# Performance work log

Hardware: AMD Instinct MI355X
Metric: run time of the kernel (lower is better)

Reference implementation:

```python
import jax, jax.numpy as jnp
import numpy as np

B, D, C, L, H = 4096, 768, 512, 32, 256
E = C * L  # total flattened extension embeddings

def _l2norm(x, eps=1e-12):
    n = jnp.sqrt(jnp.sum(x * x, axis=-1, keepdims=True))
    return x / jnp.maximum(n, eps)

def setup_inputs() -> dict:
    key = jax.random.key(0)
    ks = jax.random.split(key, 8)
    text_feat = jax.random.normal(ks[0], (B, D), dtype=jnp.float32)
    img_feat = jax.random.normal(ks[1], (B, D), dtype=jnp.float32)
    ext_embs = _l2norm(jax.random.normal(ks[2], (E, D), dtype=jnp.float32))
    concept_names = _l2norm(jax.random.normal(ks[3], (C, D), dtype=jnp.float32))
    # each concept has exactly L extension embeddings; sorted segment ids
    segment_ids = jnp.repeat(jnp.arange(C, dtype=jnp.int32), L)
    W1 = jax.random.normal(ks[4], (C + D, H), dtype=jnp.float32) * (1.0 / np.sqrt(C + D))
    b1 = jnp.zeros((H,), dtype=jnp.float32)
    W2 = jax.random.normal(ks[5], (H, C), dtype=jnp.float32) * (1.0 / np.sqrt(H))
    b2 = jnp.zeros((C,), dtype=jnp.float32)
    alpha = jnp.float32(0.5)
    temperature = jnp.float32(0.07)
    return {"text_feat": text_feat, "img_feat": img_feat, "ext_embs": ext_embs,
            "segment_ids": segment_ids, "concept_names": concept_names,
            "W1": W1, "b1": b1, "W2": W2, "b2": b2,
            "alpha": alpha, "temperature": temperature}

def reference(text_feat, img_feat, ext_embs, segment_ids, concept_names,
              W1, b1, W2, b2, alpha, temperature):
    # query = normalize(text + img)
    q = _l2norm(text_feat + img_feat)                      # [B, D]
    # ragged per-concept max similarity: one big GEMM + segmented max
    sim = jnp.einsum('bd,ed->be', q, ext_embs)            # [B, E]
    prior = jax.ops.segment_max(sim.T, segment_ids,
                                num_segments=C,
                                indices_are_sorted=True).T  # [B, C]
    # small MLP -> temperature softmax -> weighted concept sum
    h = jax.nn.relu(jnp.concatenate([prior, q], axis=-1) @ W1 + b1)  # [B, H]
    logits = h @ W2 + b2                                   # [B, C]
    weights = jax.nn.softmax(logits / temperature, axis=-1)
    dyn_prompt = weights @ concept_names                   # [B, D]
    combined = text_feat + alpha * dyn_prompt
    return _l2norm(combined)
```

## Files before the change

### kernel.cpp

```cpp
#include <hip/hip_runtime.h>
#include <hip/hip_bf16.h>

typedef unsigned short bfu;
typedef __attribute__((ext_vector_type(4))) float f32x4;
typedef __attribute__((ext_vector_type(8))) short bf16x8;
typedef __attribute__((ext_vector_type(4))) int i32x4;
typedef __attribute__((ext_vector_type(8))) int i32x8;

#define GAS __attribute__((address_space(1)))
#define LAS __attribute__((address_space(3)))

__device__ __forceinline__ unsigned short f2bf(float f) {
    unsigned int u = __float_as_uint(f);
    u += 0x7FFFu + ((u >> 16) & 1u);
    return (unsigned short)(u >> 16);
}

__device__ __forceinline__ void gld_lds16(const void* g, void* l) {
    __builtin_amdgcn_global_load_lds((GAS void*)g, (LAS void*)l, 16, 0, 0);
}

__device__ __forceinline__ unsigned pack_fp8x4(float a, float b, float c, float d) {
    int u = __builtin_amdgcn_cvt_pk_fp8_f32(a, b, 0, false);
    u = __builtin_amdgcn_cvt_pk_fp8_f32(c, d, u, true);
    return (unsigned)u;
}

__device__ __forceinline__ float block_sum256(float v, float* sm) {
    #pragma unroll
    for (int off = 32; off; off >>= 1) v += __shfl_xor(v, off);
    int w = threadIdx.x >> 6;
    if ((threadIdx.x & 63) == 0) sm[w] = v;
    __syncthreads();
    float r = sm[0] + sm[1] + sm[2] + sm[3];
    __syncthreads();
    return r;
}

__device__ __forceinline__ float block_max256(float v, float* sm) {
    #pragma unroll
    for (int off = 32; off; off >>= 1) v = fmaxf(v, __shfl_xor(v, off));
    int w = threadIdx.x >> 6;
    if ((threadIdx.x & 63) == 0) sm[w] = v;
    __syncthreads();
    float r = fmaxf(fmaxf(sm[0], sm[1]), fmaxf(sm[2], sm[3]));
    __syncthreads();
    return r;
}

__global__ __launch_bounds__(256) void prep_kernel(const float* __restrict__ text,
                                                   const float* __restrict__ img,
                                                   bfu* __restrict__ X,
                                                   unsigned* __restrict__ Q8,
                                                   const float* __restrict__ ext,
                                                   unsigned* __restrict__ E8,
                                                   const float* __restrict__ W1, bfu* __restrict__ W1t,
                                                   const float* __restrict__ W2, bfu* __restrict__ W2t,
                                                   const float* __restrict__ cn, bfu* __restrict__ cnt) {
    __shared__ float sm[4];
    int b = blockIdx.x, t = threadIdx.x;
    if (b < 4096) {
        int row = b;
        float4 v = {0.f, 0.f, 0.f, 0.f};
        if (t < 192) {
            float4 a = ((const float4*)(text + (size_t)row * 768))[t];
            float4 c = ((const float4*)(img + (size_t)row * 768))[t];
            v.x = a.x + c.x; v.y = a.y + c.y; v.z = a.z + c.z; v.w = a.w + c.w;
        }
        float ss = v.x * v.x + v.y * v.y + v.z * v.z + v.w * v.w;
        float tot = block_sum256(ss, sm);
        float inv = 1.0f / fmaxf(sqrtf(tot), 1e-12f);
        if (t < 192) {
            ushort4 o = make_ushort4(f2bf(v.x * inv), f2bf(v.y * inv), f2bf(v.z * inv), f2bf(v.w * inv));
            ((ushort4*)(X + (size_t)row * 1280 + 512))[t] = o;
            float s16 = inv * 16.0f;
            Q8[(size_t)row * 192 + t] = pack_fp8x4(v.x * s16, v.y * s16, v.z * s16, v.w * s16);
        }
    } else if (b < 16384) {
        int i = (b - 4096) * 256 + t;
        float4 v = ((const float4*)ext)[i];
        E8[i] = pack_fp8x4(v.x * 16.0f, v.y * 16.0f, v.z * 16.0f, v.w * 16.0f);
    } else if (b < 17664) {
        int idx = (b - 16384) * 256 + t;
        int c = idx / 1280, r = idx - c * 1280;
        W1t[idx] = f2bf(W1[(size_t)r * 256 + c]);
    } else if (b < 18176) {
        int idx = (b - 17664) * 256 + t;
        int c = idx / 256, r = idx - c * 256;
        W2t[idx] = f2bf(W2[(size_t)r * 512 + c]);
    } else {
        int idx = (b - 18176) * 256 + t;
        int c = idx / 512, r = idx - c * 512;
        cnt[idx] = f2bf(cn[(size_t)r * 768 + c]);
    }
}

__device__ __forceinline__ i32x8 ld_frag8(const char* s, int row, int lq) {
    const int r7 = row & 7;
    i32x4 lo = *(const i32x4*)(s + row * 128 + ((((lq << 1))     ^ r7) << 4));
    i32x4 hi = *(const i32x4*)(s + row * 128 + ((((lq << 1) | 1) ^ r7) << 4));
    i32x8 v;
    v[0] = lo[0]; v[1] = lo[1]; v[2] = lo[2]; v[3] = lo[3];
    v[4] = hi[0]; v[5] = hi[1]; v[6] = hi[2]; v[7] = hi[3];
    return v;
}

__global__ __launch_bounds__(256) void sim_segmax_kernel(const unsigned char* __restrict__ Q8,
                                                         const unsigned char* __restrict__ E8,
                                                         bfu* __restrict__ X) {
    __shared__ __align__(16) char sA[128 * 128];
    __shared__ __align__(16) char sB[128 * 128];
    int xcd = blockIdx.x & 7;
    int lid = blockIdx.x >> 3;
    int bm = lid & 31;
    int bn = ((lid >> 5) << 3) | xcd;
    int m0 = bm * 128, n0 = bn * 128;
    const int t = threadIdx.x, lane = t & 63, wv = t >> 6;
    const int wm = (wv >> 1) << 6, wn = (wv & 1) << 6;
    const int lr = lane & 15, lq = lane >> 4;

    f32x4 zero = {0.f, 0.f, 0.f, 0.f};
    f32x4 acc[4][4];
    #pragma unroll
    for (int i = 0; i < 4; ++i)
        #pragma unroll
        for (int j = 0; j < 4; ++j) acc[i][j] = zero;

    for (int k0 = 0; k0 < 768; k0 += 128) {
        #pragma unroll
        for (int i = 0; i < 4; ++i) {
            int idx = i * 256 + t;
            int row = idx >> 3, cs = idx & 7, cg = cs ^ (row & 7);
            gld_lds16(Q8 + (size_t)(m0 + row) * 768 + k0 + (cg << 4), sA + idx * 16);
            gld_lds16(E8 + (size_t)(n0 + row) * 768 + k0 + (cg << 4), sB + idx * 16);
        }
        __syncthreads();
        i32x8 af[4], bf8[4];
        #pragma unroll
        for (int f = 0; f < 4; ++f) {
            af[f]  = ld_frag8(sA, wm + f * 16 + lr, lq);
            bf8[f] = ld_frag8(sB, wn + f * 16 + lr, lq);
        }
        #pragma unroll
        for (int i = 0; i < 4; ++i)
            #pragma unroll
            for (int j = 0; j < 4; ++j)
                acc[i][j] = __builtin_amdgcn_mfma_scale_f32_16x16x128_f8f6f4(
                    af[i], bf8[j], acc[i][j], 0, 0, 0, 0x7F7F7F7F, 0, 0x7F7F7F7F);
        __syncthreads();
    }

    const float sc = 0.00390625f;
    #pragma unroll
    for (int i = 0; i < 4; ++i) {
        #pragma unroll
        for (int r = 0; r < 4; ++r) {
            float g0 = fmaxf(acc[i][0][r], acc[i][1][r]);
            float g1 = fmaxf(acc[i][2][r], acc[i][3][r]);
            #pragma unroll
            for (int off = 8; off; off >>= 1) {
                g0 = fmaxf(g0, __shfl_xor(g0, off));
                g1 = fmaxf(g1, __shfl_xor(g1, off));
            }
            if (lr == 0) {
                int row = m0 + wm + i * 16 + lq * 4 + r;
                int g = (n0 + wn) >> 5;
                X[(size_t)row * 1280 + g]     = f2bf(g0 * sc);
                X[(size_t)row * 1280 + g + 1] = f2bf(g1 * sc);
            }
        }
    }
}

template <int BM>
__device__ __forceinline__ void gemm_mainloop(const bfu* A, const bfu* B, int K,
                                              int lda, int ldb, int m0, int n0,
                                              short* sA, short* sB, f32x4 acc[BM / 32][4]) {
    const int t = threadIdx.x, lane = t & 63, wv = t >> 6;
    const int wm = (wv >> 1) * (BM / 2), wn = (wv & 1) << 6;
    const int lr = lane & 15, lq = lane >> 4;

    for (int k0 = 0; k0 < K; k0 += 64) {
        #pragma unroll
        for (int i = 0; i < BM / 32; ++i) {
            int idx = i * 256 + t;
            int row = idx >> 3, cs = idx & 7, cg = cs ^ (row & 7);
            gld_lds16(A + (size_t)(m0 + row) * lda + k0 + (cg << 3), sA + idx * 8);
        }
        #pragma unroll
        for (int i = 0; i < 4; ++i) {
            int idx = i * 256 + t;
            int row = idx >> 3, cs = idx & 7, cg = cs ^ (row & 7);
            gld_lds16(B + (size_t)(n0 + row) * ldb + k0 + (cg << 3), sB + idx * 8);
        }
        __syncthreads();
        #pragma unroll
        for (int kk = 0; kk < 2; ++kk) {
            bf16x8 af[BM / 32], bfr[4];
            #pragma unroll
            for (int f = 0; f < BM / 32; ++f) {
                int mrow = wm + f * 16 + lr;
                int c = kk * 4 + lq;
                af[f] = *(const bf16x8*)(sA + mrow * 64 + ((c ^ (mrow & 7)) << 3));
            }
            #pragma unroll
            for (int f = 0; f < 4; ++f) {
                int nrow = wn + f * 16 + lr;
                int c = kk * 4 + lq;
                bfr[f] = *(const bf16x8*)(sB + nrow * 64 + ((c ^ (nrow & 7)) << 3));
            }
            #pragma unroll
            for (int i = 0; i < BM / 32; ++i)
                #pragma unroll
                for (int j = 0; j < 4; ++j)
                    acc[i][j] = __builtin_amdgcn_mfma_f32_16x16x32_bf16(af[i], bfr[j], acc[i][j], 0, 0, 0);
        }
        __syncthreads();
    }
}

template <int EPI, int BM>
__global__ __launch_bounds__(256) void gemm_kernel(const bfu* __restrict__ A,
                                                   const bfu* __restrict__ B,
                                                   const float* __restrict__ bias,
                                                   void* __restrict__ out,
                                                   int K, int lda, int ldb, int N, int ntN) {
    __shared__ __align__(16) short sA[BM * 64];
    __shared__ __align__(16) short sB[128 * 64];
    int bm = blockIdx.x / ntN, bn = blockIdx.x - bm * ntN;
    int m0 = bm * BM, n0 = bn * 128;
    f32x4 zero = {0.f, 0.f, 0.f, 0.f};
    f32x4 acc[BM / 32][4];
    #pragma unroll
    for (int i = 0; i < BM / 32; ++i)
        #pragma unroll
        for (int j = 0; j < 4; ++j) acc[i][j] = zero;

    gemm_mainloop<BM>(A, B, K, lda, ldb, m0, n0, sA, sB, acc);

    const int t = threadIdx.x, lane = t & 63, wv = t >> 6;
    const int wm = (wv >> 1) * (BM / 2), wn = (wv & 1) << 6;
    const int lr = lane & 15, lq = lane >> 4;
    #pragma unroll
    for (int j = 0; j < 4; ++j) {
        int col = n0 + wn + j * 16 + lr;
        float bv = (EPI >= 1) ? bias[col] : 0.0f;
        #pragma unroll
        for (int i = 0; i < BM / 32; ++i) {
            #pragma unroll
            for (int r = 0; r < 4; ++r) {
                int row = m0 + wm + i * 16 + lq * 4 + r;
                float v = acc[i][j][r] + bv;
                if (EPI == 1) {
                    v = fmaxf(v, 0.0f);
                    ((bfu*)out)[(size_t)row * N + col] = f2bf(v);
                } else {
                    ((float*)out)[(size_t)row * N + col] = v;
                }
            }
        }
    }
}

__global__ __launch_bounds__(256) void softmax_kernel(const float* __restrict__ logits,
                                                      const float* __restrict__ temp,
                                                      bfu* __restrict__ wout) {
    __shared__ float sm[4];
    int row = blockIdx.x, t = threadIdx.x;
    float invT = 1.0f / temp[0];
    float l0 = logits[(size_t)row * 512 + t];
    float l1 = logits[(size_t)row * 512 + 256 + t];
    float m = block_max256(fmaxf(l0, l1), sm);
    float e0 = __expf((l0 - m) * invT);
    float e1 = __expf((l1 - m) * invT);
    float s = block_sum256(e0 + e1, sm);
    float inv = 1.0f / s;
    wout[(size_t)row * 512 + t]       = f2bf(e0 * inv);
    wout[(size_t)row * 512 + 256 + t] = f2bf(e1 * inv);
}

__global__ __launch_bounds__(256) void final_kernel(const float* __restrict__ text,
                                                    const float* __restrict__ dyn,
                                                    const float* __restrict__ alpha,
                                                    float* __restrict__ out) {
    __shared__ float sm[4];
    int row = blockIdx.x, t = threadIdx.x;
    float a = alpha[0];
    float v[3]; float ss = 0.f;
    #pragma unroll
    for (int i = 0; i < 3; ++i) {
        size_t o = (size_t)row * 768 + t + 256 * i;
        v[i] = text[o] + a * dyn[o];
        ss += v[i] * v[i];
    }
    float tot = block_sum256(ss, sm);
    float inv = 1.0f / fmaxf(sqrtf(tot), 1e-12f);
    #pragma unroll
    for (int i = 0; i < 3; ++i)
        out[(size_t)row * 768 + t + 256 * i] = v[i] * inv;
}

extern "C" void kernel_launch(void* const* d_in, const int* in_sizes, int n_in,
                              void* d_out, int out_size, void* d_ws, size_t ws_size,
                              hipStream_t stream) {
    const float* text  = (const float*)d_in[0];
    const float* img   = (const float*)d_in[1];
    const float* ext   = (const float*)d_in[2];
    const float* cn    = (const float*)d_in[4];
    const float* W1    = (const float*)d_in[5];
    const float* b1    = (const float*)d_in[6];
    const float* W2    = (const float*)d_in[7];
    const float* b2    = (const float*)d_in[8];
    const float* alpha = (const float*)d_in[9];
    const float* temp  = (const float*)d_in[10];
    float* out = (float*)d_out;

    char* p = (char*)d_ws;
    auto carve = [&](size_t bytes) -> char* {
        char* r = p; p += (bytes + 255) & ~(size_t)255; return r;
    };
    unsigned char* E8 = (unsigned char*)carve((size_t)16384 * 768);
    unsigned char* Q8 = (unsigned char*)carve((size_t)4096 * 768);
    bfu*   X      = (bfu*)carve((size_t)4096 * 1280 * 2);
    bfu*   W1t    = (bfu*)carve((size_t)256 * 1280 * 2);
    bfu*   W2t    = (bfu*)carve((size_t)512 * 256 * 2);
    bfu*   cnt    = (bfu*)carve((size_t)768 * 512 * 2);
    bfu*   Hm     = (bfu*)carve((size_t)4096 * 256 * 2);
    float* logits = (float*)carve((size_t)4096 * 512 * 4);
    bfu*   wts    = (bfu*)carve((size_t)4096 * 512 * 2);
    float* dyn    = (float*)carve((size_t)4096 * 768 * 4);

    prep_kernel<<<19712, 256, 0, stream>>>(text, img, X, (unsigned*)Q8,
                                           ext, (unsigned*)E8, W1, W1t, W2, W2t, cn, cnt);
    sim_segmax_kernel<<<4096, 256, 0, stream>>>(Q8, E8, X);
    gemm_kernel<1, 32><<<128 * 2, 256, 0, stream>>>(X, W1t, b1, (void*)Hm, 1280, 1280, 1280, 256, 2);
    gemm_kernel<2, 32><<<128 * 4, 256, 0, stream>>>(Hm, W2t, b2, (void*)logits, 256, 256, 256, 512, 4);
    softmax_kernel<<<4096, 256, 0, stream>>>(logits, temp, wts);
    gemm_kernel<0, 32><<<128 * 6, 256, 0, stream>>>(wts, cnt, nullptr, (void*)dyn, 512, 512, 512, 768, 6);
    final_kernel<<<4096, 256, 0, stream>>>(text, dyn, alpha, out);
}
```

Baseline: 314.9 us.

## Prefetch GEMM tiles through registers instead of direct global-to-LDS loads

```diff
diff --git a/kernel.cpp b/kernel.cpp
--- a/kernel.cpp
+++ b/kernel.cpp
@@ -7,17 +7,10 @@
 typedef __attribute__((ext_vector_type(4))) int i32x4;
 typedef __attribute__((ext_vector_type(8))) int i32x8;
 
-#define GAS __attribute__((address_space(1)))
-#define LAS __attribute__((address_space(3)))
-
 __device__ __forceinline__ unsigned short f2bf(float f) {
     unsigned int u = __float_as_uint(f);
     u += 0x7FFFu + ((u >> 16) & 1u);
     return (unsigned short)(u >> 16);
-}
-
-__device__ __forceinline__ void gld_lds16(const void* g, void* l) {
-    __builtin_amdgcn_global_load_lds((GAS void*)g, (LAS void*)l, 16, 0, 0);
 }
 
 __device__ __forceinline__ unsigned pack_fp8x4(float a, float b, float c, float d) {
@@ -110,10 +103,8 @@
                                                          bfu* __restrict__ X) {
     __shared__ __align__(16) char sA[128 * 128];
     __shared__ __align__(16) char sB[128 * 128];
-    int xcd = blockIdx.x & 7;
-    int lid = blockIdx.x >> 3;
-    int bm = lid & 31;
-    int bn = ((lid >> 5) << 3) | xcd;
+    int bm = blockIdx.x >> 7;
+    int bn = blockIdx.x & 127;
     int m0 = bm * 128, n0 = bn * 128;
     const int t = threadIdx.x, lane = t & 63, wv = t >> 6;
     const int wm = (wv >> 1) << 6, wn = (wv & 1) << 6;
@@ -126,15 +117,32 @@
         #pragma unroll
         for (int j = 0; j < 4; ++j) acc[i][j] = zero;
 
-    for (int k0 = 0; k0 < 768; k0 += 128) {
+    i32x4 ra[4], rb[4];
+    auto ldg = [&](int k0) {
         #pragma unroll
         for (int i = 0; i < 4; ++i) {
             int idx = i * 256 + t;
-            int row = idx >> 3, cs = idx & 7, cg = cs ^ (row & 7);
-            gld_lds16(Q8 + (size_t)(m0 + row) * 768 + k0 + (cg << 4), sA + idx * 16);
-            gld_lds16(E8 + (size_t)(n0 + row) * 768 + k0 + (cg << 4), sB + idx * 16);
-        }
+            int row = idx >> 3, cg = idx & 7;
+            ra[i] = *(const i32x4*)(Q8 + (size_t)(m0 + row) * 768 + k0 + (cg << 4));
+            rb[i] = *(const i32x4*)(E8 + (size_t)(n0 + row) * 768 + k0 + (cg << 4));
+        }
+    };
+    auto st_lds = [&]() {
+        #pragma unroll
+        for (int i = 0; i < 4; ++i) {
+            int idx = i * 256 + t;
+            int row = idx >> 3, cg = idx & 7, cs = cg ^ (row & 7);
+            *(i32x4*)(sA + (row * 8 + cs) * 16) = ra[i];
+            *(i32x4*)(sB + (row * 8 + cs) * 16) = rb[i];
+        }
+    };
+
+    ldg(0);
+    for (int kk = 0; kk < 6; ++kk) {
+        if (kk) __syncthreads();
+        st_lds();
         __syncthreads();
+        if (kk + 1 < 6) ldg((kk + 1) * 128);
         i32x8 af[4], bf8[4];
         #pragma unroll
         for (int f = 0; f < 4; ++f) {
@@ -147,7 +155,6 @@
             for (int j = 0; j < 4; ++j)
                 acc[i][j] = __builtin_amdgcn_mfma_scale_f32_16x16x128_f8f6f4(
                     af[i], bf8[j], acc[i][j], 0, 0, 0, 0x7F7F7F7F, 0, 0x7F7F7F7F);
-        __syncthreads();
     }
 
     const float sc = 0.00390625f;
@@ -180,33 +187,56 @@
     const int wm = (wv >> 1) * (BM / 2), wn = (wv & 1) << 6;
     const int lr = lane & 15, lq = lane >> 4;
 
-    for (int k0 = 0; k0 < K; k0 += 64) {
+    i32x4 ra[BM / 32], rb[4];
+    auto ldg = [&](int k0) {
         #pragma unroll
         for (int i = 0; i < BM / 32; ++i) {
             int idx = i * 256 + t;
-            int row = idx >> 3, cs = idx & 7, cg = cs ^ (row & 7);
-            gld_lds16(A + (size_t)(m0 + row) * lda + k0 + (cg << 3), sA + idx * 8);
+            int row = idx >> 3, cg = idx & 7;
+            ra[i] = *(const i32x4*)(A + (size_t)(m0 + row) * lda + k0 + (cg << 3));
         }
         #pragma unroll
         for (int i = 0; i < 4; ++i) {
             int idx = i * 256 + t;
-            int row = idx >> 3, cs = idx & 7, cg = cs ^ (row & 7);
-            gld_lds16(B + (size_t)(n0 + row) * ldb + k0 + (cg << 3), sB + idx * 8);
-        }
+            int row = idx >> 3, cg = idx & 7;
+            rb[i] = *(const i32x4*)(B + (size_t)(n0 + row) * ldb + k0 + (cg << 3));
+        }
+    };
+    auto st_lds = [&]() {
+        #pragma unroll
+        for (int i = 0; i < BM / 32; ++i) {
+            int idx = i * 256 + t;
+            int row = idx >> 3, cg = idx & 7, cs = cg ^ (row & 7);
+            *(i32x4*)(sA + row * 64 + cs * 8) = ra[i];
+        }
+        #pragma unroll
+        for (int i = 0; i < 4; ++i) {
+            int idx = i * 256 + t;
+            int row = idx >> 3, cg = idx & 7, cs = cg ^ (row & 7);
+            *(i32x4*)(sB + row * 64 + cs * 8) = rb[i];
+        }
+    };
+
+    const int NIT = K >> 6;
+    ldg(0);
+    for (int kk = 0; kk < NIT; ++kk) {
+        if (kk) __syncthreads();
+        st_lds();
         __syncthreads();
-        #pragma unroll
-        for (int kk = 0; kk < 2; ++kk) {
+        if (kk + 1 < NIT) ldg((kk + 1) * 64);
+        #pragma unroll
+        for (int ks = 0; ks < 2; ++ks) {
             bf16x8 af[BM / 32], bfr[4];
             #pragma unroll
             for (int f = 0; f < BM / 32; ++f) {
                 int mrow = wm + f * 16 + lr;
-                int c = kk * 4 + lq;
+                int c = ks * 4 + lq;
                 af[f] = *(const bf16x8*)(sA + mrow * 64 + ((c ^ (mrow & 7)) << 3));
             }
             #pragma unroll
             for (int f = 0; f < 4; ++f) {
                 int nrow = wn + f * 16 + lr;
-                int c = kk * 4 + lq;
+                int c = ks * 4 + lq;
                 bfr[f] = *(const bf16x8*)(sB + nrow * 64 + ((c ^ (nrow & 7)) << 3));
             }
             #pragma unroll
@@ -215,7 +245,6 @@
                 for (int j = 0; j < 4; ++j)
                     acc[i][j] = __builtin_amdgcn_mfma_f32_16x16x32_bf16(af[i], bfr[j], acc[i][j], 0, 0, 0);
         }
-        __syncthreads();
     }
 }
 
```

Result: faster. 301.4 us (-4.3%).
